# Kernel optimization log

Hardware: AMD Instinct MI355X
Metric: run time of the kernel (lower is better)

Reference implementation:

```python
import jax, jax.numpy as jnp
import numpy as np

N_POINTS = 300000
NUM_CLUSTERS = 64
LATENT_DIM = 32
DET = 1e-16  # matches `det` in update_gamma


def setup_inputs() -> dict:
    key = jax.random.key(0)
    k1, k2, k3 = jax.random.split(key, 3)
    mu_phi = jax.random.normal(k1, (N_POINTS, LATENT_DIM), dtype=jnp.float32)
    # per-node scalar log-variance (encoder's gcn_logstddev has output dim 1)
    log_cov_phi = jax.random.normal(k2, (N_POINTS, 1), dtype=jnp.float32) * 0.1
    pi_k = jnp.ones((NUM_CLUSTERS,), jnp.float32) / NUM_CLUSTERS
    mu_k = jax.random.normal(k3, (NUM_CLUSTERS, LATENT_DIM), dtype=jnp.float32)
    log_cov_k = jnp.full((NUM_CLUSTERS, 1), 0.1, jnp.float32)
    return {"mu_phi": mu_phi, "log_cov_phi": log_cov_phi, "pi_k": pi_k,
            "mu_k": mu_k, "log_cov_k": log_cov_k, "P": LATENT_DIM}


def _sq_dist(a, b):
    # ||a_i - b_k||^2 via expansion; avoids materializing [N,K,P]
    return (jnp.sum(a * a, axis=1)[:, None]
            - 2.0 * (a @ b.T)
            + jnp.sum(b * b, axis=1)[None, :])


def reference(mu_phi, log_cov_phi, pi_k, mu_k, log_cov_k, P):
    Pf = jnp.float32(P)
    lcp = log_cov_phi[:, 0]          # [N]
    lck = log_cov_k[:, 0]            # [K]
    # --- update_gamma: KL[i,k] between q(z_i) and cluster k (isotropic) ---
    sq = _sq_dist(mu_phi, mu_k)      # [N,K]
    inv_cov_k = jnp.exp(-lck)[None, :]
    KL = 0.5 * (Pf * (lck[None, :] - lcp[:, None]) - Pf
                + Pf * jnp.exp(lcp)[:, None] * inv_cov_k
                + sq * inv_cov_k)    # [N,K]
    w = pi_k[None, :] * jnp.exp(-KL)
    gamma = w / jnp.sum(w, axis=1, keepdims=True) + DET  # [N,K]
    # --- update_others: M-step using the new gamma ---
    N_k = jnp.sum(gamma, axis=0)                          # [K]
    pi_new = N_k / jnp.float32(gamma.shape[0])
    mu_new = (gamma.T @ mu_phi) / N_k[:, None]            # [K,P]
    sq2 = _sq_dist(mu_phi, mu_new)                        # [N,K]
    diff = Pf * jnp.exp(lcp)[:, None] + sq2               # [N,K]
    cov_new = jnp.sum(gamma * diff, axis=0) / (Pf * N_k)  # [K]
    log_cov_new = jnp.log(cov_new)[:, None]               # [K,1]
    return gamma, pi_new, mu_new, log_cov_new
```

## Files before the change

### kernel.cpp

```cpp
#include <hip/hip_runtime.h>
#include <math.h>

#define NPTS 300000
#define K 64
#define P 32
#define DETC 1e-16f
#define WS_FLOATS (K + K + K * P)

#define NBLOCKS 1024
#define NTHREADS 256
#define NWAVES (NBLOCKS * (NTHREADS / 64))
#define CHUNK ((NPTS + NWAVES - 1) / NWAVES)

#define DPP_ADD(v, ctrl)                                                     \
    v += __int_as_float(__builtin_amdgcn_update_dpp(                         \
        0, __float_as_int(v), (ctrl), 0xF, 0xF, true))

__device__ __forceinline__ float rl(float x, int lane) {
    return __int_as_float(__builtin_amdgcn_readlane(__float_as_int(x), lane));
}

__global__ __launch_bounds__(NTHREADS, 4) void em_pass(
    const float* __restrict__ mu_phi,
    const float* __restrict__ log_cov_phi,
    const float* __restrict__ pi_k,
    const float* __restrict__ mu_k,
    const float* __restrict__ log_cov_k,
    float* __restrict__ gamma_out,
    float* __restrict__ out_tail,
    float* __restrict__ ws)
{
    const int lane = threadIdx.x & 63;
    const int wave = threadIdx.x >> 6;
    const int gw = __builtin_amdgcn_readfirstlane(blockIdx.x * (NTHREADS / 64) + wave);

    float muk[P];
#pragma unroll
    for (int d = 0; d < P; ++d) muk[d] = mu_k[lane * P + d];
    const float lck  = log_cov_k[lane];
    const float icov = __expf(-lck);
    const float pik  = pi_k[lane];
    float n2k = 0.f;
#pragma unroll
    for (int d = 0; d < P; ++d) n2k = fmaf(muk[d], muk[d], n2k);
    const float Ak    = 0.5f * (32.f * lck - 32.f + icov * n2k) - __logf(pik);
    const float hicov = 0.5f * icov;

    float accN = 0.f, accS = 0.f;
    float accM[P];
#pragma unroll
    for (int d = 0; d < P; ++d) accM[d] = 0.f;

    const int start = gw * CHUNK;
    const int end0  = (start + CHUNK < NPTS) ? (start + CHUNK) : NPTS;

    for (int gb = start; gb < end0; gb += 64) {
        const int cnt = (end0 - gb < 64) ? (end0 - gb) : 64;

        float u_v = 0.f, lcp_v = 0.f;
        const int ip = gb + lane;
        if (lane < cnt) {
            const float4* r4 = reinterpret_cast<const float4*>(mu_phi + (size_t)ip * P);
            float4 a0 = r4[0], a1 = r4[1], a2 = r4[2], a3 = r4[3];
            float4 a4 = r4[4], a5 = r4[5], a6 = r4[6], a7 = r4[7];
            float n2 = 0.f;
#define N2ACC(q) n2 = fmaf(q.x,q.x,n2); n2 = fmaf(q.y,q.y,n2); \
                 n2 = fmaf(q.z,q.z,n2); n2 = fmaf(q.w,q.w,n2)
            N2ACC(a0); N2ACC(a1); N2ACC(a2); N2ACC(a3);
            N2ACC(a4); N2ACC(a5); N2ACC(a6); N2ACC(a7);
#undef N2ACC
            lcp_v = log_cov_phi[ip];
            u_v   = fmaf(32.f, __expf(lcp_v), n2);
        }

#pragma unroll 2
        for (int p = 0; p < cnt; ++p) {
            const int i = gb + p;
            const float u_s    = rl(u_v, p);
            const float base_s = 16.f * rl(lcp_v, p);
            const float* row = mu_phi + (size_t)i * P;

            float dot = 0.f;
#pragma unroll
            for (int d = 0; d < P; ++d) dot = fmaf(row[d], muk[d], dot);

            const float t = fmaf(-hicov, u_s, base_s) - Ak;
            const float w = __expf(fmaf(icov, dot, t));

            float v = w;
            DPP_ADD(v, 0xB1);
            DPP_ADD(v, 0x4E);
            DPP_ADD(v, 0x128);
            DPP_ADD(v, 0x124);
            const float sum = (rl(v, 0) + rl(v, 16)) + (rl(v, 32) + rl(v, 48));

            const float g = fmaf(w, __builtin_amdgcn_rcpf(sum), DETC);
            gamma_out[(size_t)i * K + lane] = g;

            accN += g;
            accS  = fmaf(g, u_s, accS);
#pragma unroll
            for (int d = 0; d < P; ++d) accM[d] = fmaf(g, row[d], accM[d]);
        }
    }

    __shared__ float lN[K], lS[K], lM[K * P];
    for (int idx = threadIdx.x; idx < K; idx += NTHREADS) { lN[idx] = 0.f; lS[idx] = 0.f; }
    for (int idx = threadIdx.x; idx < K * P; idx += NTHREADS) lM[idx] = 0.f;
    __syncthreads();

    atomicAdd(&lN[lane], accN);
    atomicAdd(&lS[lane], accS);
#pragma unroll
    for (int d = 0; d < P; ++d) atomicAdd(&lM[d * K + lane], accM[d]);
    __syncthreads();

    for (int idx = threadIdx.x; idx < K; idx += NTHREADS) {
        atomicAdd(&ws[idx], lN[idx]);
        atomicAdd(&ws[K + idx], lS[idx]);
    }
    for (int idx = threadIdx.x; idx < K * P; idx += NTHREADS)
        atomicAdd(&ws[2 * K + idx], lM[idx]);
    __syncthreads();

    __shared__ int lastf;
    if (threadIdx.x == 0) {
        __threadfence();
        const int c = atomicAdd((int*)(ws + WS_FLOATS), 1);
        lastf = (c == NBLOCKS - 1);
    }
    __syncthreads();
    if (lastf) {
        __threadfence();
        const int k = threadIdx.x;
        if (k < K) {
            const float Nk = __hip_atomic_load(&ws[k],     __ATOMIC_RELAXED, __HIP_MEMORY_SCOPE_AGENT);
            const float S  = __hip_atomic_load(&ws[K + k], __ATOMIC_RELAXED, __HIP_MEMORY_SCOPE_AGENT);
            float* pi_new      = out_tail;
            float* mu_new      = out_tail + K;
            float* log_cov_new = out_tail + K + K * P;

            pi_new[k] = Nk / (float)NPTS;
            const float invN = 1.f / Nk;
            float m2 = 0.f;
#pragma unroll
            for (int d = 0; d < P; ++d) {
                const float md = __hip_atomic_load(&ws[2 * K + d * K + k],
                                                   __ATOMIC_RELAXED, __HIP_MEMORY_SCOPE_AGENT) * invN;
                mu_new[k * P + d] = md;
                m2 = fmaf(md, md, m2);
            }
            const float cov = (S - Nk * m2) / (32.f * Nk);
            log_cov_new[k] = logf(cov);
        }
    }
}

extern "C" void kernel_launch(void* const* d_in, const int* in_sizes, int n_in,
                              void* d_out, int out_size, void* d_ws, size_t ws_size,
                              hipStream_t stream)
{
    const float* mu_phi      = (const float*)d_in[0];
    const float* log_cov_phi = (const float*)d_in[1];
    const float* pi_k        = (const float*)d_in[2];
    const float* mu_k        = (const float*)d_in[3];
    const float* log_cov_k   = (const float*)d_in[4];
    float* out = (float*)d_out;
    float* ws  = (float*)d_ws;

    hipMemsetAsync(ws, 0, (WS_FLOATS + 1) * sizeof(float), stream);
    em_pass<<<NBLOCKS, NTHREADS, 0, stream>>>(mu_phi, log_cov_phi, pi_k, mu_k,
                                              log_cov_k, out,
                                              out + (size_t)NPTS * K, ws);
}
```

Measured before the change: 203.7 us.

## Assign one 64-point tile per wave and broadcast rows via readlane

Launches one wave per 64-point tile, about 4688 waves, instead of 4096 waves each looping over a multi-tile chunk. Each lane loads one point's row into registers, and the inner loop broadcasts that row with readlane instead of reloading it from memory, so the repeated scalar/global loads in the inner loop go away. The dot product now uses four partial accumulators, and the wave sum finishes with row-broadcast DPP steps plus a single readlane. In exchange, many more blocks each do the per-block shared and global atomic reduction, and the 32 readlanes per point add SALU/VALU work.

```diff
diff --git a/kernel.cpp b/kernel.cpp
--- a/kernel.cpp
+++ b/kernel.cpp
@@ -7,17 +7,28 @@
 #define DETC 1e-16f
 #define WS_FLOATS (K + K + K * P)
 
-#define NBLOCKS 1024
 #define NTHREADS 256
-#define NWAVES (NBLOCKS * (NTHREADS / 64))
-#define CHUNK ((NPTS + NWAVES - 1) / NWAVES)
+#define WPB (NTHREADS / 64)
+#define NTILES ((NPTS + 63) / 64)
+#define NBLOCKS ((NTILES + WPB - 1) / WPB)
 
 #define DPP_ADD(v, ctrl)                                                     \
     v += __int_as_float(__builtin_amdgcn_update_dpp(                         \
         0, __float_as_int(v), (ctrl), 0xF, 0xF, true))
 
-__device__ __forceinline__ float rl(float x, int lane) {
-    return __int_as_float(__builtin_amdgcn_readlane(__float_as_int(x), lane));
+__device__ __forceinline__ float rlf(float x, int l) {
+    return __int_as_float(__builtin_amdgcn_readlane(__float_as_int(x), l));
+}
+
+__device__ __forceinline__ float wave_sum64(float w) {
+    float v = w;
+    DPP_ADD(v, 0xB1);
+    DPP_ADD(v, 0x4E);
+    DPP_ADD(v, 0x128);
+    DPP_ADD(v, 0x124);
+    DPP_ADD(v, 0x142);
+    DPP_ADD(v, 0x143);
+    return rlf(v, 63);
 }
 
 __global__ __launch_bounds__(NTHREADS, 4) void em_pass(
@@ -32,7 +43,7 @@
 {
     const int lane = threadIdx.x & 63;
     const int wave = threadIdx.x >> 6;
-    const int gw = __builtin_amdgcn_readfirstlane(blockIdx.x * (NTHREADS / 64) + wave);
+    const int tile = __builtin_amdgcn_readfirstlane(blockIdx.x * WPB + wave);
 
     float muk[P];
 #pragma unroll
@@ -51,56 +62,56 @@
 #pragma unroll
     for (int d = 0; d < P; ++d) accM[d] = 0.f;
 
-    const int start = gw * CHUNK;
-    const int end0  = (start + CHUNK < NPTS) ? (start + CHUNK) : NPTS;
+    if (tile < NTILES) {
+        const int gb  = tile * 64;
+        const int cnt = (NPTS - gb < 64) ? (NPTS - gb) : 64;
 
-    for (int gb = start; gb < end0; gb += 64) {
-        const int cnt = (end0 - gb < 64) ? (end0 - gb) : 64;
-
-        float u_v = 0.f, lcp_v = 0.f;
-        const int ip = gb + lane;
-        if (lane < cnt) {
+        const int ip = gb + ((lane < cnt) ? lane : (cnt - 1));
+        float r[P];
+        {
             const float4* r4 = reinterpret_cast<const float4*>(mu_phi + (size_t)ip * P);
             float4 a0 = r4[0], a1 = r4[1], a2 = r4[2], a3 = r4[3];
             float4 a4 = r4[4], a5 = r4[5], a6 = r4[6], a7 = r4[7];
-            float n2 = 0.f;
-#define N2ACC(q) n2 = fmaf(q.x,q.x,n2); n2 = fmaf(q.y,q.y,n2); \
-                 n2 = fmaf(q.z,q.z,n2); n2 = fmaf(q.w,q.w,n2)
-            N2ACC(a0); N2ACC(a1); N2ACC(a2); N2ACC(a3);
-            N2ACC(a4); N2ACC(a5); N2ACC(a6); N2ACC(a7);
-#undef N2ACC
-            lcp_v = log_cov_phi[ip];
-            u_v   = fmaf(32.f, __expf(lcp_v), n2);
+#define PUT(j,q) r[4*j+0]=q.x; r[4*j+1]=q.y; r[4*j+2]=q.z; r[4*j+3]=q.w
+            PUT(0,a0); PUT(1,a1); PUT(2,a2); PUT(3,a3);
+            PUT(4,a4); PUT(5,a5); PUT(6,a6); PUT(7,a7);
+#undef PUT
         }
+        float n2 = 0.f;
+#pragma unroll
+        for (int d = 0; d < P; ++d) n2 = fmaf(r[d], r[d], n2);
+        const float lcp = log_cov_phi[ip];
+        const float u_v = fmaf(32.f, __expf(lcp), n2);
+        const float b_v = 16.f * lcp;
 
-#pragma unroll 2
         for (int p = 0; p < cnt; ++p) {
-            const int i = gb + p;
-            const float u_s    = rl(u_v, p);
-            const float base_s = 16.f * rl(lcp_v, p);
-            const float* row = mu_phi + (size_t)i * P;
+            float sr[P];
+#pragma unroll
+            for (int d = 0; d < P; ++d) sr[d] = rlf(r[d], p);
 
-            float dot = 0.f;
+            float d0 = 0.f, d1 = 0.f, d2 = 0.f, d3 = 0.f;
 #pragma unroll
-            for (int d = 0; d < P; ++d) dot = fmaf(row[d], muk[d], dot);
+            for (int d = 0; d < P; d += 4) {
+                d0 = fmaf(sr[d + 0], muk[d + 0], d0);
+                d1 = fmaf(sr[d + 1], muk[d + 1], d1);
+                d2 = fmaf(sr[d + 2], muk[d + 2], d2);
+                d3 = fmaf(sr[d + 3], muk[d + 3], d3);
+            }
+            const float dot = (d0 + d1) + (d2 + d3);
 
-            const float t = fmaf(-hicov, u_s, base_s) - Ak;
+            const float u_s = rlf(u_v, p);
+            const float b_s = rlf(b_v, p);
+            const float t = fmaf(-hicov, u_s, b_s) - Ak;
             const float w = __expf(fmaf(icov, dot, t));
 
-            float v = w;
-            DPP_ADD(v, 0xB1);
-            DPP_ADD(v, 0x4E);
-            DPP_ADD(v, 0x128);
-            DPP_ADD(v, 0x124);
-            const float sum = (rl(v, 0) + rl(v, 16)) + (rl(v, 32) + rl(v, 48));
-
-            const float g = fmaf(w, __builtin_amdgcn_rcpf(sum), DETC);
-            gamma_out[(size_t)i * K + lane] = g;
+            const float s = wave_sum64(w);
+            const float g = fmaf(w, __builtin_amdgcn_rcpf(s), DETC);
+            gamma_out[(size_t)(gb + p) * K + lane] = g;
 
             accN += g;
-            accS  = fmaf(g, u_s, accS);
+            accS = fmaf(g, u_s, accS);
 #pragma unroll
-            for (int d = 0; d < P; ++d) accM[d] = fmaf(g, row[d], accM[d]);
+            for (int d = 0; d < P; ++d) accM[d] = fmaf(g, sr[d], accM[d]);
         }
     }
 
```

Result: slower. 216.2 us (+6.2%).
